# Optimization experiments

Hardware: AMD Instinct MI355X
Metric: run time of the kernel (lower is better)

Reference implementation:

```python
import jax, jax.numpy as jnp
import numpy as np

HEADS = 16
DIM_HEAD = 64
NUM_W = 4  # num_adaptive_weights
SCALE = DIM_HEAD ** -0.5


def setup_inputs() -> dict:
    key = jax.random.key(0)
    k0, k1, k2, k3 = jax.random.split(key, 4)
    b, n, dim = 2, 2048, 1024
    dim_inner = HEADS * DIM_HEAD  # 1024
    x = jax.random.normal(k0, (b, n, dim), jnp.float32)
    # Linear weights stored as (in, out); torch Linear(in,out,bias=False) computes x @ W.T
    Wqkv = jax.random.normal(k1, (dim, dim_inner * 3 * NUM_W), jnp.float32) * (dim ** -0.5)
    Wg = jax.random.normal(k2, (dim, NUM_W), jnp.float32) * (dim ** -0.5)
    Wout = jax.random.normal(k3, (dim_inner, dim * NUM_W), jnp.float32) * (dim_inner ** -0.5)
    mask = jnp.ones((b, n), dtype=bool)
    return {"x": x, "Wqkv": Wqkv, "Wg": Wg, "Wout": Wout, "mask": mask}


def reference(x, Wqkv, Wg, Wout, mask):
    b, n, dim = x.shape
    # to_qkv: packed last dim order is (qkv, h, d, w) per Rearrange 'b n (qkv h d w) -> qkv b h n d w'
    qkv = (x @ Wqkv).reshape(b, n, 3, HEADS, DIM_HEAD, NUM_W)
    qkv = jnp.transpose(qkv, (2, 0, 3, 1, 4, 5))  # [3, b, h, n, d, w]
    # adaptive gates: softmax over the w adaptive weights
    gates = jax.nn.softmax(x @ Wg, axis=-1)  # [b, n, w]
    # gated sum over adaptive-weight axis
    qkv = jnp.einsum('qbhndw,bnw->qbhnd', qkv, gates)
    q, k, v = qkv[0] * SCALE, qkv[1], qkv[2]
    sim = jnp.einsum('bhid,bhjd->bhij', q, k)  # [b, h, n, n]
    sim = jnp.where(mask[:, None, None, :], sim, jnp.finfo(sim.dtype).min)
    attn = jax.nn.softmax(sim, axis=-1)
    out = jnp.einsum('bhij,bhjd->bhid', attn, v)  # [b, h, n, d]
    out = out.transpose(0, 2, 1, 3).reshape(b, n, HEADS * DIM_HEAD)  # 'b h n d -> b n (h d)'
    out = (out @ Wout).reshape(b, n, dim, NUM_W)  # 'b n (d w) -> b n d w'
    # gated sum over w for the output projection
    return jnp.einsum('bndw,bnw->bnd', out, gates)
```

## Files before the change

### kernel.cpp

```cpp
#include <hip/hip_runtime.h>
#include <hip/hip_bf16.h>

#define M_TOT 4096
#define DIM_  1024
#define KP    4096
#define NC1   3072
#define NC2   1024

typedef unsigned short u16;
typedef unsigned int u32;
typedef unsigned long long u64;
typedef short bf16x8 __attribute__((ext_vector_type(8)));
typedef float f32x4 __attribute__((ext_vector_type(4)));

#define QSCALE 0.18033688011112042f
#define EXPOFF 20.0f

static __device__ __forceinline__ u16 f2bf(float f) {
    union { float f; u32 u; } v; v.f = f;
    u32 u = v.u;
    u += 0x7fffu + ((u >> 16) & 1u);
    return (u16)(u >> 16);
}
static __device__ __forceinline__ float bf2f(u16 h) {
    union { u32 u; float f; } v; v.u = ((u32)h) << 16; return v.f;
}

static __device__ __forceinline__ void gld_lds16(const u16* g, u16* l) {
    __builtin_amdgcn_global_load_lds(
        (__attribute__((address_space(1))) void*)(u64)g,
        (__attribute__((address_space(3))) void*)(u32)(u64)l,
        16, 0, 0);
}

#define SWZ_SCOL(lane) ((((lane) & 7) ^ (((lane) >> 3) & 7)) * 8)

#define RAW_BARRIER()   asm volatile("s_barrier" ::: "memory")
#define WAIT_VM0()      asm volatile("s_waitcnt vmcnt(0)" ::: "memory")
#define WAIT_VM4()      asm volatile("s_waitcnt vmcnt(4)" ::: "memory")
#define WAIT_VM8()      asm volatile("s_waitcnt vmcnt(8)" ::: "memory")
#define WAIT_LGKM0()    asm volatile("s_waitcnt lgkmcnt(0)" ::: "memory")

__global__ __launch_bounds__(256) void gates_expand_kernel(const float* __restrict__ x,
                                                           const float* __restrict__ Wg,
                                                           float* __restrict__ gates,
                                                           u16* __restrict__ outA) {
    const int wid = threadIdx.x >> 6, lane = threadIdx.x & 63;
    const int m = blockIdx.x * 4 + wid;
    const float* xr = x + (size_t)m * DIM_;
    float a0 = 0.f, a1 = 0.f, a2 = 0.f, a3 = 0.f;
    for (int i = 0; i < DIM_ / 64; ++i) {
        int k = i * 64 + lane;
        float xv = xr[k];
        float4 wg = ((const float4*)Wg)[k];
        a0 += xv * wg.x; a1 += xv * wg.y; a2 += xv * wg.z; a3 += xv * wg.w;
    }
    for (int s = 1; s < 64; s <<= 1) {
        a0 += __shfl_xor(a0, s); a1 += __shfl_xor(a1, s);
        a2 += __shfl_xor(a2, s); a3 += __shfl_xor(a3, s);
    }
    float mx = fmaxf(fmaxf(a0, a1), fmaxf(a2, a3));
    float e0 = __expf(a0 - mx), e1 = __expf(a1 - mx), e2 = __expf(a2 - mx), e3 = __expf(a3 - mx);
    float inv = 1.0f / (e0 + e1 + e2 + e3);
    float g0 = e0 * inv, g1 = e1 * inv, g2 = e2 * inv, g3 = e3 * inv;
    if (lane == 0) ((float4*)gates)[m] = make_float4(g0, g1, g2, g3);
    ushort4* out4 = (ushort4*)outA;
    for (int i = 0; i < DIM_ / 64; ++i) {
        int k = i * 64 + lane;
        float val = xr[k];
        ushort4 o;
        o.x = f2bf(val * g0); o.y = f2bf(val * g1); o.z = f2bf(val * g2); o.w = f2bf(val * g3);
        out4[(size_t)m * 1024 + k] = o;
    }
}

__global__ __launch_bounds__(256) void bprep_kernel(const float* __restrict__ src,
                                                    u16* __restrict__ dst,
                                                    int R, int Cg) {
    __shared__ u16 lds[64 * 68];
    const int t = threadIdx.x;
    const int cg0 = blockIdx.x * 16, k0 = blockIdx.y * 64;
    const float4* s4 = (const float4*)src;
    for (int i = 0; i < 4; ++i) {
        int f = i * 256 + t;
        int kl = f >> 4, f4 = f & 15;
        float4 v = s4[(size_t)(k0 + kl) * Cg + cg0 + f4];
        ushort4 o; o.x = f2bf(v.x); o.y = f2bf(v.y); o.z = f2bf(v.z); o.w = f2bf(v.w);
        *(ushort4*)&lds[kl * 68 + f4 * 4] = o;
    }
    __syncthreads();
    ushort4* d4 = (ushort4*)dst;
    for (int i = 0; i < 4; ++i) {
        int j = i * 256 + t;
        int cgl = j >> 6, kl = j & 63;
        d4[(size_t)(cg0 + cgl) * R + k0 + kl] = *(ushort4*)&lds[kl * 68 + cgl * 4];
    }
}

__global__ __launch_bounds__(512, 2) void gemm1_kernel(const u16* __restrict__ A,
                                                       const u16* __restrict__ Bm,
                                                       u16* __restrict__ qbuf,
                                                       u16* __restrict__ kbuf,
                                                       u16* __restrict__ vbuf) {
    __shared__ u16 lA[4][256 * 32];
    __shared__ u16 lB[4][256 * 32];
    const int t = threadIdx.x;
    const int lane = t & 63, wid = t >> 6;
    const int wm = wid >> 2, wn = wid & 3;
    const int l15 = lane & 15, quad = lane >> 4;
    const int sw = (l15 >> 1) & 3;
    const int n0 = blockIdx.x * 256, m0 = blockIdx.y * 256;
    const int srow = lane >> 2;
    const int scol = (((lane & 3) ^ ((lane >> 3) & 3)) * 8);
    const u16* gA = A + (size_t)(m0 + wid * 32 + srow) * KP + scol;
    const u16* gB = Bm + (size_t)(n0 + wid * 32 + srow) * KP + scol;
    u16* lAw = &lA[0][0] + wid * 32 * 32;
    u16* lBw = &lB[0][0] + wid * 32 * 32;

#define G1_STAGE(tt) do {                                              \
        const int _s = (tt) & 3;                                       \
        const size_t _k = (size_t)(tt) * 32;                           \
        gld_lds16(gA + _k,                    lAw + _s * 8192);        \
        gld_lds16(gA + _k + (size_t)16 * KP,  lAw + _s * 8192 + 512);  \
        gld_lds16(gB + _k,                    lBw + _s * 8192);        \
        gld_lds16(gB + _k + (size_t)16 * KP,  lBw + _s * 8192 + 512);  \
    } while (0)

    f32x4 acc[8][4] = {};
    G1_STAGE(0); G1_STAGE(1); G1_STAGE(2);
    const int co = (quad ^ sw) * 8;
    for (int kt = 0; kt < 128; ++kt) {
        if (kt < 126)      WAIT_VM8();
        else if (kt == 126) WAIT_VM4();
        else               WAIT_VM0();
        RAW_BARRIER();
        if (kt < 125) G1_STAGE(kt + 3);
        const u16* sA = &lA[kt & 3][0];
        const u16* sB = &lB[kt & 3][0];
        bf16x8 af[8], bfr[4];
#pragma unroll
        for (int mt = 0; mt < 8; ++mt)
            af[mt] = *(const bf16x8*)&sA[(wm * 128 + mt * 16 + l15) * 32 + co];
#pragma unroll
        for (int nt = 0; nt < 4; ++nt)
            bfr[nt] = *(const bf16x8*)&sB[(wn * 64 + nt * 16 + l15) * 32 + co];
        __builtin_amdgcn_s_setprio(1);
#pragma unroll
        for (int mt = 0; mt < 8; ++mt)
#pragma unroll
            for (int nt = 0; nt < 4; ++nt)
                acc[mt][nt] = __builtin_amdgcn_mfma_f32_16x16x32_bf16(af[mt], bfr[nt], acc[mt][nt], 0, 0, 0);
        __builtin_amdgcn_s_setprio(0);
    }
#undef G1_STAGE

    const int qkv = n0 >> 10;
    const int base_hd = n0 & 1023;
    for (int mt = 0; mt < 8; ++mt) {
        int mrow = m0 + wm * 128 + mt * 16 + quad * 4;
        int b = mrow >> 11, n = mrow & 2047;
        int bh0 = b * 16;
        for (int nt = 0; nt < 4; ++nt) {
            int hd = base_hd + wn * 64 + nt * 16 + l15;
            int h = hd >> 6, d = hd & 63;
            int bh = bh0 + h;
            if (qkv == 0) {
                for (int r = 0; r < 4; ++r)
                    qbuf[((size_t)bh * 2048 + n + r) * 64 + d] = f2bf(acc[mt][nt][r] * QSCALE);
            } else if (qkv == 1) {
                for (int r = 0; r < 4; ++r)
                    kbuf[((size_t)bh * 2048 + n + r) * 64 + d] = f2bf(acc[mt][nt][r]);
            } else {
                ushort4 o;
                o.x = f2bf(acc[mt][nt][0]); o.y = f2bf(acc[mt][nt][1]);
                o.z = f2bf(acc[mt][nt][2]); o.w = f2bf(acc[mt][nt][3]);
                *(ushort4*)&vbuf[((size_t)bh * 64 + d) * 2048 + n] = o;
            }
        }
    }
}

__global__ __launch_bounds__(256) void gemm2_kernel(const u16* __restrict__ A,
                                                    const u16* __restrict__ Bm,
                                                    float* __restrict__ outf) {
    __shared__ u16 lA[2][128 * 64];
    __shared__ u16 lB[2][64 * 64];
    const int t = threadIdx.x;
    const int lane = t & 63, wid = t >> 6;
    const int wm = wid >> 1, wn = wid & 1;
    const int l15 = lane & 15, quad = lane >> 4;
    const int sx = l15 & 7;
    const int n0 = blockIdx.x * 64, m0 = blockIdx.y * 128;
    const int srow = lane >> 3, scol = SWZ_SCOL(lane);
    const u16* gA = A + (size_t)(m0 + wid * 32 + srow) * KP + scol;
    const u16* gB = Bm + (size_t)(n0 + wid * 16 + srow) * KP + scol;
    for (int i = 0; i < 4; ++i)
        gld_lds16(gA + (size_t)i * 8 * KP, &lA[0][(wid * 32 + i * 8) * 64]);
    for (int i = 0; i < 2; ++i)
        gld_lds16(gB + (size_t)i * 8 * KP, &lB[0][(wid * 16 + i * 8) * 64]);
    f32x4 acc[4][2] = {};
    for (int it = 0; it < 64; ++it) {
        const int cur = it & 1;
        WAIT_VM0();
        RAW_BARRIER();
        if (it + 1 < 64) {
            const int k0 = (it + 1) * 64, nb = cur ^ 1;
            for (int i = 0; i < 4; ++i)
                gld_lds16(gA + (size_t)i * 8 * KP + k0, &lA[nb][(wid * 32 + i * 8) * 64]);
            for (int i = 0; i < 2; ++i)
                gld_lds16(gB + (size_t)i * 8 * KP + k0, &lB[nb][(wid * 16 + i * 8) * 64]);
        }
        for (int ks = 0; ks < 2; ++ks) {
            const int co = ((ks * 4 + quad) ^ sx) * 8;
            bf16x8 af[4], bfr[2];
            for (int mt = 0; mt < 4; ++mt)
                af[mt] = *(const bf16x8*)&lA[cur][(wm * 64 + mt * 16 + l15) * 64 + co];
            for (int nt = 0; nt < 2; ++nt)
                bfr[nt] = *(const bf16x8*)&lB[cur][(wn * 32 + nt * 16 + l15) * 64 + co];
            for (int mt = 0; mt < 4; ++mt)
                for (int nt = 0; nt < 2; ++nt)
                    acc[mt][nt] = __builtin_amdgcn_mfma_f32_16x16x32_bf16(af[mt], bfr[nt], acc[mt][nt], 0, 0, 0);
        }
    }
    for (int mt = 0; mt < 4; ++mt) {
        int mrow = m0 + wm * 64 + mt * 16 + quad * 4;
        for (int nt = 0; nt < 2; ++nt) {
            int col = n0 + wn * 32 + nt * 16 + l15;
            for (int r = 0; r < 4; ++r)
                outf[(size_t)(mrow + r) * NC2 + col] = acc[mt][nt][r];
        }
    }
}

__global__ __launch_bounds__(256) void attn_kernel(const u16* __restrict__ qbuf,
                                                   const u16* __restrict__ kbuf,
                                                   const u16* __restrict__ vbuf,
                                                   const float* __restrict__ gates,
                                                   u16* __restrict__ outA) {
    __shared__ u16 lK[2][64 * 64];
    __shared__ u16 lV[2][64 * 64];
    __shared__ u16 lP[4][2 * 16 * 72];
    const int t = threadIdx.x, lane = t & 63, wq = t >> 6;
    const int l15 = lane & 15, quad = lane >> 4;
    const int sx7 = l15 & 7;
    const int bh = blockIdx.y, q0 = blockIdx.x * 128;
    const u16* Q = qbuf + (size_t)bh * 2048 * 64;
    const u16* K = kbuf + (size_t)bh * 2048 * 64;
    const u16* V = vbuf + (size_t)bh * 64 * 2048;
    bf16x8 qf[2][2];
    for (int mt = 0; mt < 2; ++mt)
        for (int ks = 0; ks < 2; ++ks)
            qf[mt][ks] = *(const bf16x8*)&Q[(size_t)(q0 + wq * 32 + mt * 16 + l15) * 64 + ks * 32 + quad * 8];
    f32x4 Oa[2][4] = {};
    float lacc[2] = {0.f, 0.f};
    const int krow = lane >> 3, kcol = SWZ_SCOL(lane);
    const u16* gK = K + (size_t)(wq * 16 + krow) * 64 + kcol;
    const u16* gV = V + (size_t)(wq * 16 + krow) * 2048 + kcol;
    u16* lPw = lP[wq];
    gld_lds16(gK, &lK[0][(wq * 16) * 64]);
    gld_lds16(gK + (size_t)8 * 64, &lK[0][(wq * 16 + 8) * 64]);
    gld_lds16(gV, &lV[0][(wq * 16) * 64]);
    gld_lds16(gV + (size_t)8 * 2048, &lV[0][(wq * 16 + 8) * 64]);
    for (int kt = 0; kt < 32; ++kt) {
        const int cur = kt & 1;
        WAIT_VM0();
        RAW_BARRIER();
        if (kt + 1 < 32) {
            const int nxt = (kt + 1) * 64, nb = cur ^ 1;
            gld_lds16(gK + (size_t)nxt * 64, &lK[nb][(wq * 16) * 64]);
            gld_lds16(gK + (size_t)(nxt + 8) * 64, &lK[nb][(wq * 16 + 8) * 64]);
            gld_lds16(gV + nxt, &lV[nb][(wq * 16) * 64]);
            gld_lds16(gV + nxt + (size_t)8 * 2048, &lV[nb][(wq * 16 + 8) * 64]);
        }
        f32x4 S[2][4] = {};
        for (int ks = 0; ks < 2; ++ks) {
            const int co = ((ks * 4 + quad) ^ sx7) * 8;
            for (int nt = 0; nt < 4; ++nt) {
                bf16x8 kf = *(const bf16x8*)&lK[cur][(nt * 16 + l15) * 64 + co];
                S[0][nt] = __builtin_amdgcn_mfma_f32_16x16x32_bf16(kf, qf[0][ks], S[0][nt], 0, 0, 0);
                S[1][nt] = __builtin_amdgcn_mfma_f32_16x16x32_bf16(kf, qf[1][ks], S[1][nt], 0, 0, 0);
            }
        }
        for (int mt = 0; mt < 2; ++mt) {
            u16* lPm = lPw + mt * (16 * 72);
            for (int nt = 0; nt < 4; ++nt) {
                float p0 = __builtin_amdgcn_exp2f(S[mt][nt][0] - EXPOFF);
                float p1 = __builtin_amdgcn_exp2f(S[mt][nt][1] - EXPOFF);
                float p2 = __builtin_amdgcn_exp2f(S[mt][nt][2] - EXPOFF);
                float p3 = __builtin_amdgcn_exp2f(S[mt][nt][3] - EXPOFF);
                lacc[mt] += (p0 + p1) + (p2 + p3);
                uint2 pk;
                pk.x = (u32)f2bf(p0) | ((u32)f2bf(p1) << 16);
                pk.y = (u32)f2bf(p2) | ((u32)f2bf(p3) << 16);
                *(uint2*)&lPm[l15 * 72 + nt * 16 + quad * 4] = pk;
            }
        }
        WAIT_LGKM0();
        for (int ks = 0; ks < 2; ++ks) {
            const int co = ((ks * 4 + quad) ^ sx7) * 8;
            bf16x8 p0 = *(const bf16x8*)&lPw[0 * (16 * 72) + l15 * 72 + ks * 32 + quad * 8];
            bf16x8 p1 = *(const bf16x8*)&lPw[1 * (16 * 72) + l15 * 72 + ks * 32 + quad * 8];
            for (int dt = 0; dt < 4; ++dt) {
                bf16x8 vf = *(const bf16x8*)&lV[cur][(dt * 16 + l15) * 64 + co];
                Oa[0][dt] = __builtin_amdgcn_mfma_f32_16x16x32_bf16(p0, vf, Oa[0][dt], 0, 0, 0);
                Oa[1][dt] = __builtin_amdgcn_mfma_f32_16x16x32_bf16(p1, vf, Oa[1][dt], 0, 0, 0);
            }
        }
    }
    for (int mt = 0; mt < 2; ++mt) {
        lacc[mt] += __shfl_xor(lacc[mt], 16);
        lacc[mt] += __shfl_xor(lacc[mt], 32);
    }
    const int b = bh >> 4, h = bh & 15;
    ushort4* out4 = (ushort4*)outA;
    const float4* gates4 = (const float4*)gates;
    for (int mt = 0; mt < 2; ++mt) {
        for (int r = 0; r < 4; ++r) {
            int n = q0 + wq * 32 + mt * 16 + quad * 4 + r;
            int m = b * 2048 + n;
            float invl = 1.0f / __shfl(lacc[mt], quad * 4 + r);
            float4 g = gates4[m];
            for (int dt = 0; dt < 4; ++dt) {
                float val = Oa[mt][dt][r] * invl;
                ushort4 o;
                o.x = f2bf(val * g.x); o.y = f2bf(val * g.y);
                o.z = f2bf(val * g.z); o.w = f2bf(val * g.w);
                out4[(size_t)m * 1024 + h * 64 + dt * 16 + l15] = o;
            }
        }
    }
}

extern "C" void kernel_launch(void* const* d_in, const int* in_sizes, int n_in,
                              void* d_out, int out_size, void* d_ws, size_t ws_size,
                              hipStream_t stream) {
    const float* x    = (const float*)d_in[0];
    const float* Wqkv = (const float*)d_in[1];
    const float* Wg   = (const float*)d_in[2];
    const float* Wout = (const float*)d_in[3];

    char* ws = (char*)d_ws;
    size_t off = 0;
    float* gates = (float*)(ws + off); off += (size_t)1 << 16;
    u16* Aexp = (u16*)(ws + off);      off += (size_t)M_TOT * KP * 2;
    char* regB = ws + off;             off += (size_t)NC1 * KP * 2;
    u16* B1 = (u16*)regB;
    u16* B2 = (u16*)(regB + (size_t)M_TOT * NC2 * 2);
    u16* qbuf = (u16*)(ws + off); off += (size_t)32 * 2048 * 64 * 2;
    u16* kbuf = (u16*)(ws + off); off += (size_t)32 * 2048 * 64 * 2;
    u16* vbuf = (u16*)(ws + off); off += (size_t)32 * 2048 * 64 * 2;

    hipLaunchKernelGGL(gates_expand_kernel, dim3(1024), dim3(256), 0, stream,
                       x, Wg, gates, Aexp);
    hipLaunchKernelGGL(bprep_kernel, dim3(192, 16), dim3(256), 0, stream,
                       Wqkv, B1, 1024, 3072);
    hipLaunchKernelGGL(gemm1_kernel, dim3(12, 16), dim3(512), 0, stream,
                       Aexp, B1, qbuf, kbuf, vbuf);
    hipLaunchKernelGGL(bprep_kernel, dim3(64, 16), dim3(256), 0, stream,
                       Wout, B2, 1024, 1024);
    hipLaunchKernelGGL(attn_kernel, dim3(16, 32), dim3(256), 0, stream,
                       qbuf, kbuf, vbuf, gates, Aexp);
    hipLaunchKernelGGL(gemm2_kernel, dim3(16, 32), dim3(256), 0, stream,
                       Aexp, B2, (float*)d_out);
}
```

Before: 392.5 us.

## Split gemm1 k-step into two half-phases interleaving LDS reads, prefetch and MFMA

Restructures the gemm1 main loop into two phases per k-tile. Each phase loads half of the A fragments, issues half of the next-stage global-to-LDS prefetch (A or B) and runs half of the MFMAs, with extra barriers and LDS waits, in a ping-pong style schedule. Launch bounds drop from 2 blocks to 1 block per CU, which frees registers. The aim is to overlap memory traffic with matrix math more evenly, at the cost of more barriers per iteration and lower occupancy.

```diff
diff --git a/kernel.cpp b/kernel.cpp
--- a/kernel.cpp
+++ b/kernel.cpp
@@ -97,7 +97,7 @@
     }
 }
 
-__global__ __launch_bounds__(512, 2) void gemm1_kernel(const u16* __restrict__ A,
+__global__ __launch_bounds__(512, 1) void gemm1_kernel(const u16* __restrict__ A,
                                                        const u16* __restrict__ Bm,
                                                        u16* __restrict__ qbuf,
                                                        u16* __restrict__ kbuf,
@@ -114,45 +114,71 @@
     const int scol = (((lane & 3) ^ ((lane >> 3) & 3)) * 8);
     const u16* gA = A + (size_t)(m0 + wid * 32 + srow) * KP + scol;
     const u16* gB = Bm + (size_t)(n0 + wid * 32 + srow) * KP + scol;
-    u16* lAw = &lA[0][0] + wid * 32 * 32;
-    u16* lBw = &lB[0][0] + wid * 32 * 32;
-
-#define G1_STAGE(tt) do {                                              \
+    u16* lAw = &lA[0][0] + wid * 1024;
+    u16* lBw = &lB[0][0] + wid * 1024;
+
+#define G1_STAGE_A(tt) do {                                            \
         const int _s = (tt) & 3;                                       \
         const size_t _k = (size_t)(tt) * 32;                           \
         gld_lds16(gA + _k,                    lAw + _s * 8192);        \
         gld_lds16(gA + _k + (size_t)16 * KP,  lAw + _s * 8192 + 512);  \
+    } while (0)
+#define G1_STAGE_B(tt) do {                                            \
+        const int _s = (tt) & 3;                                       \
+        const size_t _k = (size_t)(tt) * 32;                           \
         gld_lds16(gB + _k,                    lBw + _s * 8192);        \
         gld_lds16(gB + _k + (size_t)16 * KP,  lBw + _s * 8192 + 512);  \
     } while (0)
 
     f32x4 acc[8][4] = {};
-    G1_STAGE(0); G1_STAGE(1); G1_STAGE(2);
+    G1_STAGE_A(0); G1_STAGE_B(0);
+    G1_STAGE_A(1); G1_STAGE_B(1);
+    G1_STAGE_A(2); G1_STAGE_B(2);
+    WAIT_VM8();
+    RAW_BARRIER();
     const int co = (quad ^ sw) * 8;
     for (int kt = 0; kt < 128; ++kt) {
-        if (kt < 126)      WAIT_VM8();
-        else if (kt == 126) WAIT_VM4();
-        else               WAIT_VM0();
-        RAW_BARRIER();
-        if (kt < 125) G1_STAGE(kt + 3);
         const u16* sA = &lA[kt & 3][0];
         const u16* sB = &lB[kt & 3][0];
-        bf16x8 af[8], bfr[4];
-#pragma unroll
-        for (int mt = 0; mt < 8; ++mt)
-            af[mt] = *(const bf16x8*)&sA[(wm * 128 + mt * 16 + l15) * 32 + co];
+        bf16x8 afA[4], bfr[4];
+#pragma unroll
+        for (int mt = 0; mt < 4; ++mt)
+            afA[mt] = *(const bf16x8*)&sA[(wm * 128 + mt * 16 + l15) * 32 + co];
 #pragma unroll
         for (int nt = 0; nt < 4; ++nt)
             bfr[nt] = *(const bf16x8*)&sB[(wn * 64 + nt * 16 + l15) * 32 + co];
+        if (kt < 125) G1_STAGE_A(kt + 3);
+        RAW_BARRIER();
+        WAIT_LGKM0();
         __builtin_amdgcn_s_setprio(1);
 #pragma unroll
-        for (int mt = 0; mt < 8; ++mt)
+        for (int mt = 0; mt < 4; ++mt)
 #pragma unroll
             for (int nt = 0; nt < 4; ++nt)
-                acc[mt][nt] = __builtin_amdgcn_mfma_f32_16x16x32_bf16(af[mt], bfr[nt], acc[mt][nt], 0, 0, 0);
+                acc[mt][nt] = __builtin_amdgcn_mfma_f32_16x16x32_bf16(afA[mt], bfr[nt], acc[mt][nt], 0, 0, 0);
         __builtin_amdgcn_s_setprio(0);
-    }
-#undef G1_STAGE
+        RAW_BARRIER();
+        bf16x8 afB[4];
+#pragma unroll
+        for (int mt = 0; mt < 4; ++mt)
+            afB[mt] = *(const bf16x8*)&sA[(wm * 128 + (mt + 4) * 16 + l15) * 32 + co];
+        if (kt < 125) G1_STAGE_B(kt + 3);
+        RAW_BARRIER();
+        WAIT_LGKM0();
+        __builtin_amdgcn_s_setprio(1);
+#pragma unroll
+        for (int mt = 0; mt < 4; ++mt)
+#pragma unroll
+            for (int nt = 0; nt < 4; ++nt)
+                acc[mt + 4][nt] = __builtin_amdgcn_mfma_f32_16x16x32_bf16(afB[mt], bfr[nt], acc[mt + 4][nt], 0, 0, 0);
+        __builtin_amdgcn_s_setprio(0);
+        if (kt < 125)       WAIT_VM8();
+        else if (kt == 125) WAIT_VM4();
+        else if (kt == 126) WAIT_VM0();
+        RAW_BARRIER();
+    }
+#undef G1_STAGE_A
+#undef G1_STAGE_B
 
     const int qkv = n0 >> 10;
     const int base_hd = n0 & 1023;
```

Measured after the change: 386.6 us. Within noise of the previous version (-1.5%).
